# Kernel optimization log

Hardware: AMD Instinct MI355X
Metric: run time of the kernel (lower is better)

Reference implementation:

```python
import jax, jax.numpy as jnp
import numpy as np

EPS = 1e-8
LN_EPS = 1e-5
TOPK = 8

B, N, D = 8, 2048, 512


def setup_inputs() -> dict:
    key = jax.random.key(0)
    ks = jax.random.split(key, 4)
    feats = jax.random.normal(ks[0], (B, N, D), dtype=jnp.float32)
    mask = jnp.ones((B, N), dtype=bool)
    # per-layer GCN weights (no bias) and LayerNorm params, plus output LN
    W1 = jax.random.normal(ks[1], (D, D), dtype=jnp.float32) / np.sqrt(D)
    W2 = jax.random.normal(ks[2], (D, D), dtype=jnp.float32) / np.sqrt(D)
    ln1_g = jnp.ones((D,), jnp.float32); ln1_b = jnp.zeros((D,), jnp.float32)
    ln2_g = jnp.ones((D,), jnp.float32); ln2_b = jnp.zeros((D,), jnp.float32)
    out_g = jnp.ones((D,), jnp.float32); out_b = jnp.zeros((D,), jnp.float32)
    return {"feats": feats, "mask": mask, "W1": W1, "ln1_g": ln1_g, "ln1_b": ln1_b,
            "W2": W2, "ln2_g": ln2_g, "ln2_b": ln2_b, "out_g": out_g, "out_b": out_b}


def _layer_norm(x, g, b):
    mu = jnp.mean(x, axis=-1, keepdims=True)
    var = jnp.mean(jnp.square(x - mu), axis=-1, keepdims=True)
    return (x - mu) * jax.lax.rsqrt(var + LN_EPS) * g + b


def build_similarity_graph(feats, mask):
    b, n, _ = feats.shape
    mask_f = mask.astype(feats.dtype)                       # [B,N]
    valid_pair = mask[:, None, :] & mask[:, :, None]        # [B,N,N]
    vp_f = valid_pair.astype(feats.dtype)
    # cosine similarity mapped to [0,1]
    fn = feats / jnp.clip(jnp.linalg.norm(feats, axis=-1, keepdims=True), EPS)
    sim = (jnp.einsum('bnd,bmd->bnm', fn, fn) + 1.0) * 0.5
    sim = sim * vp_f
    eye = jnp.eye(n, dtype=bool)
    sim_wo_self = jnp.where(eye[None], 0.0, sim)
    # top-k neighbors per node (invalid pairs pushed to -1)
    k = min(TOPK, n - 1)
    candidate = jnp.where(valid_pair, sim_wo_self, -1.0)
    values, indices = jax.lax.top_k(candidate, k)           # [B,N,k]
    bi = jnp.arange(b)[:, None, None]
    ri = jnp.arange(n)[None, :, None]
    knn_mask = jnp.zeros((b, n, n), dtype=bool).at[bi, ri, indices].set(values > 0)
    adj = sim_wo_self * knn_mask.astype(feats.dtype)
    # symmetrize, add valid self-loops, re-mask
    adj = 0.5 * (adj + jnp.swapaxes(adj, 1, 2))
    adj = adj + jnp.eye(n, dtype=feats.dtype)[None] * (mask_f[:, :, None] * mask_f[:, None, :])
    adj = adj * vp_f
    # symmetric degree normalization
    deg_inv_sqrt = jnp.clip(adj.sum(-1), EPS) ** -0.5       # [B,N]
    adj_norm = adj * deg_inv_sqrt[:, :, None] * deg_inv_sqrt[:, None, :]
    return adj_norm * vp_f


def _gcn_layer(x, adj_norm, W, g, b, mask_f):
    out = jnp.einsum('bnm,bmd->bnd', adj_norm, x @ W) + x   # residual (Identity proj)
    out = jax.nn.relu(_layer_norm(out, g, b))
    return out * mask_f[..., None]


def reference(feats, mask, W1, ln1_g, ln1_b, W2, ln2_g, ln2_b, out_g, out_b):
    mask_f = mask.astype(feats.dtype)
    x = feats * mask_f[..., None]                           # input_proj = Identity, then mask
    adj_norm = build_similarity_graph(feats, mask)
    x = _gcn_layer(x, adj_norm, W1, ln1_g, ln1_b, mask_f)
    x = _gcn_layer(x, adj_norm, W2, ln2_g, ln2_b, mask_f)
    x = _layer_norm(x, out_g, out_b)
    return x * mask_f[..., None]
```

## Files before the change

kernel.cpp:

```cpp
#include <hip/hip_runtime.h>
#include <cstdint>


constexpr int Bb   = 8;
constexpr int Nn   = 2048;
constexpr int Dd   = 512;
constexpr int BN   = Bb * Nn;
constexpr int KTOP = 8;
constexpr int CAP  = 56;
constexpr int NSLICE = 8;

typedef __attribute__((ext_vector_type(8))) __bf16 bf16x8;
typedef __attribute__((ext_vector_type(4))) __bf16 bf16x4;
typedef __attribute__((ext_vector_type(4))) float  f32x4;

__device__ __forceinline__ void gload16(const void* g, void* l) {
  __builtin_amdgcn_global_load_lds((const __attribute__((address_space(1))) unsigned int*)g,
                                   (__attribute__((address_space(3))) unsigned int*)l,
                                   16, 0, 0);
}
__device__ __forceinline__ void barrier_raw() {
  asm volatile("" ::: "memory");
  __builtin_amdgcn_s_barrier();
  asm volatile("" ::: "memory");
}
__device__ __forceinline__ unsigned umax_(unsigned a, unsigned b) { return a > b ? a : b; }
__device__ __forceinline__ unsigned umin_(unsigned a, unsigned b) { return a > b ? b : a; }

__global__ __launch_bounds__(256) void prep_kernel(const float* __restrict__ feats,
                                                   float* __restrict__ rinv,
                                                   float* __restrict__ normv,
                                                   __bf16* __restrict__ Hk,
                                                   int* __restrict__ ecnt,
                                                   const float* __restrict__ W1,
                                                   const float* __restrict__ W2,
                                                   __bf16* __restrict__ Wk1,
                                                   __bf16* __restrict__ Wk2) {
  __shared__ float tile[64][65];
  __shared__ float rsh[64];
  const int t = threadIdx.x;

  if (blockIdx.x >= 256) {
    const int idx = blockIdx.x - 256;
    const float* W = (idx >> 8) ? W2 : W1;
    __bf16* Wk     = (idx >> 8) ? Wk2 : Wk1;
    const int rem = idx & 255;
    const int bx = (rem & 15) * 32, by = (rem >> 4) * 32;
    float (*tt)[33] = (float(*)[33])tile;
    const int lx = t & 31, ly = t >> 5;
#pragma unroll
    for (int r = 0; r < 32; r += 8)
      tt[ly + r][lx] = W[(size_t)(by + ly + r) * Dd + bx + lx];
    __syncthreads();
    if (t < 128) {
      const int k8l = t >> 5, nl = t & 31;
      bf16x8 v;
#pragma unroll
      for (int e = 0; e < 8; ++e) v[e] = (__bf16)tt[k8l * 8 + e][nl];
      *(bf16x8*)(Wk + ((size_t)((by >> 3) + k8l) * Dd + bx + nl) * 8) = v;
    }
    return;
  }

  const int r0 = blockIdx.x * 64;
  const int bz = r0 >> 11;
  const int n0 = r0 & 2047;
  const int wv = t >> 6, lane = t & 63;

  if (t < 64) ecnt[r0 + t] = 0;

  for (int i = 0; i < 16; ++i) {
    const int row = wv * 16 + i;
    const float* p = feats + (size_t)(r0 + row) * Dd + lane * 8;
    float4 a = *(const float4*)p;
    float4 b = *(const float4*)(p + 4);
    float s = a.x*a.x + a.y*a.y + a.z*a.z + a.w*a.w
            + b.x*b.x + b.y*b.y + b.z*b.z + b.w*b.w;
#pragma unroll
    for (int o = 32; o; o >>= 1) s += __shfl_down(s, o);
    if (lane == 0) {
      const float nr = fmaxf(sqrtf(s), 1e-8f);
      rsh[row] = 1.0f / nr;
      rinv[r0 + row]  = 1.0f / nr;
      normv[r0 + row] = nr;
    }
  }

  for (int kt = 0; kt < 8; ++kt) {
    __syncthreads();
#pragma unroll
    for (int p = 0; p < 4; ++p) {
      const int row = p * 16 + (t >> 4), ch = t & 15;
      float4 v = *(const float4*)(feats + (size_t)(r0 + row) * Dd + kt * 64 + ch * 4);
      tile[row][ch * 4 + 0] = v.x; tile[row][ch * 4 + 1] = v.y;
      tile[row][ch * 4 + 2] = v.z; tile[row][ch * 4 + 3] = v.w;
    }
    __syncthreads();
#pragma unroll
    for (int h = 0; h < 2; ++h) {
      const int c = h * 256 + t;
      const int k8l = c >> 6, row = c & 63;
      const float s = rsh[row];
      bf16x8 hv;
#pragma unroll
      for (int e = 0; e < 8; ++e) hv[e] = (__bf16)(tile[row][k8l * 8 + e] * s);
      *(bf16x8*)(Hk + ((size_t)(bz * 64) + (size_t)(kt * 8 + k8l)) * (Nn * 8)
                    + (n0 + row) * 8) = hv;
    }
  }
}

__device__ __forceinline__ void ins8t(float (&tv)[8], int (&ti)[8], float v, int idx) {
#pragma unroll
  for (int q = 0; q < 8; ++q) {
    bool sw = (v > tv[q]) || (v == tv[q] && idx < ti[q]);
    float a = sw ? tv[q] : v;
    int   c = sw ? ti[q] : idx;
    tv[q] = sw ? v   : tv[q];
    ti[q] = sw ? idx : ti[q];
    v = a; idx = c;
  }
}

__device__ __forceinline__ void gemm_core(const __bf16* __restrict__ Ab, int Astr, int mloc,
                                          const __bf16* __restrict__ Wk, int m0, int n0,
                                          __bf16* __restrict__ Yb, int tid, char* smem) {
  const int lane   = tid & 63;
  const int lane15 = tid & 15;
  const int kgrp   = (tid >> 4) & 3;
  const int wv     = tid >> 6;
  const int wrow0  = wv * 32;

  auto stage = [&](int t, int buf) {
    const int k80 = t << 2;
#pragma unroll
    for (int i = 0; i < 4; ++i) {
      const int c = (wv << 2) + i;
      const bool isB = c >= 8;
      const int cc = isB ? c - 8 : c;
      const int kg = cc >> 1, rb = cc & 1;
      const __bf16* g = isB
          ? Wk + ((size_t)(k80 + kg) * Dd + n0 + rb * 64 + lane) * 8
          : Ab + ((size_t)(k80 + kg) * Astr + mloc + rb * 64 + lane) * 8;
      gload16(g, smem + buf * 16384 + (isB ? 8192 : 0) + kg * 2048 + (rb * 64 + lane) * 16);
    }
  };

  f32x4 acc[2][8];
  const f32x4 z = {0.f, 0.f, 0.f, 0.f};
#pragma unroll
  for (int i = 0; i < 2; ++i)
#pragma unroll
    for (int j = 0; j < 8; ++j) acc[i][j] = z;

  stage(0, 0);
  for (int t = 0; t < 16; ++t) {
    const int cur = t & 1;
    if (t + 1 < 16) {
      stage(t + 1, cur ^ 1);
      asm volatile("s_waitcnt vmcnt(4)" ::: "memory");
    } else {
      asm volatile("s_waitcnt vmcnt(0)" ::: "memory");
    }
    barrier_raw();

    const char* sb = smem + cur * 16384;
    const int a0o = kgrp * 2048 + (wrow0 + lane15) * 16;
    bf16x8 a0 = *(const bf16x8*)(sb + a0o);
    bf16x8 a1 = *(const bf16x8*)(sb + a0o + 256);
#pragma unroll
    for (int cs = 0; cs < 8; ++cs) {
      bf16x8 b = *(const bf16x8*)(sb + 8192 + kgrp * 2048 + (cs * 16 + lane15) * 16);
      acc[0][cs] = __builtin_amdgcn_mfma_f32_16x16x32_bf16(b, a0, acc[0][cs], 0, 0, 0);
      acc[1][cs] = __builtin_amdgcn_mfma_f32_16x16x32_bf16(b, a1, acc[1][cs], 0, 0, 0);
    }
    barrier_raw();
  }
#pragma unroll
  for (int rs = 0; rs < 2; ++rs) {
    const int row = m0 + wv * 32 + rs * 16 + lane15;
#pragma unroll
    for (int cs = 0; cs < 8; ++cs) {
      bf16x4 o;
#pragma unroll
      for (int e = 0; e < 4; ++e) o[e] = (__bf16)acc[rs][cs][e];
      *(bf16x4*)(Yb + (size_t)row * Dd + n0 + cs * 16 + kgrp * 4) = o;
    }
  }
}

__global__ __launch_bounds__(256, 4) void sim_gemm_kernel(const __bf16* __restrict__ Hk,
                                                          const __bf16* __restrict__ Wk1,
                                                          __bf16* __restrict__ Yb,
                                                          float* __restrict__ pv,
                                                          int* __restrict__ pi) {
  __shared__ __align__(16) char smem[32768];
  const int tid = threadIdx.x;

  if (blockIdx.x < 512) {
    const int gb = blockIdx.x;
    const int m0 = (gb >> 2) * 128, n0 = (gb & 3) * 128;
    const __bf16* Ab = Hk + (size_t)((m0 >> 11) * 64) * (Nn * 8);
    gemm_core(Ab, Nn, m0 & 2047, Wk1, m0, n0, Yb, tid, smem);
    return;
  }

  const int f     = blockIdx.x - 512;
  const int bz    = f & 7;
  const int rr    = f >> 3;
  const int r0    = (rr & 15) * 128;
  const int slice = rr >> 4;

  const int lane   = tid & 63;
  const int lane15 = tid & 15;
  const int kgrp   = (tid >> 4) & 3;
  const int wv     = tid >> 6;
  const int wrow0  = wv * 32;
  const int bN     = bz * Nn;

  const __bf16* Hb = Hk + (size_t)(bz * 64) * (Nn * 8);

  unsigned t8k[2][8];
#pragma unroll
  for (int rs = 0; rs < 2; ++rs)
#pragma unroll
    for (int q = 0; q < 8; ++q) t8k[rs][q] = 0u;

  auto stage = [&](int t, int buf) {
    const int ct = t >> 4, k80 = (t & 15) << 2;
    const int c0 = slice * 256 + ct * 128;
#pragma unroll
    for (int i = 0; i < 4; ++i) {
      const int c = (wv << 2) + i;
      const bool isB = c >= 8;
      const int cc = isB ? c - 8 : c;
      const int kg = cc >> 1, rb = cc & 1;
      const int rbase = (isB ? c0 : r0) + rb * 64 + lane;
      gload16(Hb + ((size_t)(k80 + kg) * Nn + rbase) * 8,
              smem + buf * 16384 + (isB ? 8192 : 0) + kg * 2048 + (rb * 64 + lane) * 16);
    }
  };

  f32x4 acc[2][8];
  const f32x4 z = {0.f, 0.f, 0.f, 0.f};

  stage(0, 0);
  for (int t = 0; t < 32; ++t) {
    const int cur = t & 1;
    if ((t & 15) == 0) {
#pragma unroll
      for (int i = 0; i < 2; ++i)
#pragma unroll
        for (int j = 0; j < 8; ++j) acc[i][j] = z;
    }
    if (t + 1 < 32) {
      stage(t + 1, cur ^ 1);
      asm volatile("s_waitcnt vmcnt(4)" ::: "memory");
    } else {
      asm volatile("s_waitcnt vmcnt(0)" ::: "memory");
    }
    barrier_raw();

    const char* sb = smem + cur * 16384;
    const int a0o = kgrp * 2048 + (wrow0 + lane15) * 16;
    bf16x8 ah0 = *(const bf16x8*)(sb + a0o);
    bf16x8 ah1 = *(const bf16x8*)(sb + a0o + 256);
#pragma unroll
    for (int cs = 0; cs < 8; ++cs) {
      bf16x8 bh = *(const bf16x8*)(sb + 8192 + kgrp * 2048 + (cs * 16 + lane15) * 16);
      acc[0][cs] = __builtin_amdgcn_mfma_f32_16x16x32_bf16(bh, ah0, acc[0][cs], 0, 0, 0);
      acc[1][cs] = __builtin_amdgcn_mfma_f32_16x16x32_bf16(bh, ah1, acc[1][cs], 0, 0, 0);
    }
    barrier_raw();

    if ((t & 15) == 15) {
      const int ctile0 = slice * 256 + (t >> 4) * 128;
#pragma unroll
      for (int rs = 0; rs < 2; ++rs) {
        const int rowg = r0 + wrow0 + rs * 16 + lane15;
#pragma unroll
        for (int cs = 0; cs < 8; ++cs) {
          const int colb = ctile0 + cs * 16 + kgrp * 4;
#pragma unroll
          for (int e = 0; e < 4; ++e) {
            const int col = colb + e;
            unsigned key = (__float_as_uint(acc[rs][cs][e] + 2.0f) & 0xFFFFF800u)
                         | (unsigned)(0x7FF - col);
            key = (col == rowg) ? 0u : key;
#pragma unroll
            for (int q = 0; q < 8; ++q) {
              const unsigned hi = umax_(t8k[rs][q], key);
              key = umin_(t8k[rs][q], key);
              t8k[rs][q] = hi;
            }
          }
        }
      }
    }
  }

#pragma unroll
  for (int rs = 0; rs < 2; ++rs) {
#pragma unroll
    for (int m = 16; m <= 32; m <<= 1) {
      unsigned ok[8];
#pragma unroll
      for (int q = 0; q < 8; ++q) ok[q] = (unsigned)__shfl_xor((int)t8k[rs][q], m);
#pragma unroll
      for (int q = 0; q < 8; ++q) {
        unsigned key = ok[q];
#pragma unroll
        for (int p = 0; p < 8; ++p) {
          const unsigned hi = umax_(t8k[rs][p], key);
          key = umin_(t8k[rs][p], key);
          t8k[rs][p] = hi;
        }
      }
    }
  }

  if (lane < 16) {
#pragma unroll
    for (int rs = 0; rs < 2; ++rs) {
      const int prow = bN + r0 + wrow0 + rs * 16 + lane15;
#pragma unroll
      for (int q = 0; q < 8; ++q) {
        const unsigned key = t8k[rs][q];
        const int col = 0x7FF - (int)(key & 0x7FFu);
        const float raw = __uint_as_float(key & 0xFFFFF800u) - 2.0f;
        pv[((size_t)prow * NSLICE + slice) * 8 + q] = fmaxf((raw + 1.0f) * 0.5f, 0.0f);
        pi[((size_t)prow * NSLICE + slice) * 8 + q] = bN + col;
      }
    }
  }
}

__global__ __launch_bounds__(256, 4) void gemm2_kernel(const __bf16* __restrict__ Ak,
                                                       const __bf16* __restrict__ Wk,
                                                       __bf16* __restrict__ Yb) {
  __shared__ __align__(16) char smem[32768];
  const int gb = blockIdx.x;
  const int m0 = (gb >> 2) * 128, n0 = (gb & 3) * 128;
  gemm_core(Ak, BN, m0, Wk, m0, n0, Yb, threadIdx.x, smem);
}

__global__ __launch_bounds__(256) void refine_edges(const float* __restrict__ feats,
                                                    const float* __restrict__ rinv,
                                                    const float* __restrict__ pv,
                                                    const int* __restrict__ pi,
                                                    int* __restrict__ ecnt,
                                                    int* __restrict__ eidx,
                                                    float* __restrict__ ew) {
  const int f  = blockIdx.x;
  const int bz = f & 7;
  const int wv = threadIdx.x >> 6;
  const int lane = threadIdx.x & 63;
  const int bN = bz * Nn;
  const int row = bN + (f >> 3) * 4 + wv;

  const float scr = pv[(size_t)row * 64 + lane];
  const int   sid = pi[(size_t)row * 64 + lane];
  unsigned key = (__float_as_uint(scr) & 0xFFFFF800u) | (unsigned)(0x7FF - (sid - bN));

  const float* xi = feats + (size_t)row * Dd + lane * 8;
  const float4 xi0 = *(const float4*)xi;
  const float4 xi1 = *(const float4*)(xi + 4);
  const float  ri  = rinv[row];

  int ridx[12];
#pragma unroll
  for (int c = 0; c < 12; ++c) {
    unsigned m = key;
#pragma unroll
    for (int o = 32; o; o >>= 1) {
      const unsigned om = __shfl_xor(m, o);
      m = om > m ? om : m;
    }
    if (key == m) key = 0u;
    ridx[c] = bN + (0x7FF - (int)(m & 0x7FFu));
  }

  float rv[12];
#pragma unroll
  for (int c = 0; c < 12; c += 2) {
    const float* xa = feats + (size_t)ridx[c]     * Dd + lane * 8;
    const float* xb = feats + (size_t)ridx[c + 1] * Dd + lane * 8;
    const float4 a0 = *(const float4*)xa;
    const float4 a1 = *(const float4*)(xa + 4);
    const float4 b0 = *(const float4*)xb;
    const float4 b1 = *(const float4*)(xb + 4);
    float da = xi0.x*a0.x + xi0.y*a0.y + xi0.z*a0.z + xi0.w*a0.w
             + xi1.x*a1.x + xi1.y*a1.y + xi1.z*a1.z + xi1.w*a1.w;
    float db = xi0.x*b0.x + xi0.y*b0.y + xi0.z*b0.z + xi0.w*b0.w
             + xi1.x*b1.x + xi1.y*b1.y + xi1.z*b1.z + xi1.w*b1.w;
#pragma unroll
    for (int o = 32; o; o >>= 1) { da += __shfl_xor(da, o); db += __shfl_xor(db, o); }
    rv[c]     = (da * ri * rinv[ridx[c]]     + 1.0f) * 0.5f;
    rv[c + 1] = (db * ri * rinv[ridx[c + 1]] + 1.0f) * 0.5f;
  }

  float t8v[8]; int t8i[8];
#pragma unroll
  for (int q = 0; q < 8; ++q) { t8v[q] = -1.0f; t8i[q] = 0x7fffffff; }
#pragma unroll
  for (int c = 0; c < 12; ++c) ins8t(t8v, t8i, rv[c], ridx[c]);

  if (lane == 0) {
#pragma unroll
    for (int q = 0; q < KTOP; ++q) {
      if (t8v[q] > 0.0f) {
        const int j = t8i[q];
        const float w = 0.5f * t8v[q];
        int p = atomicAdd(&ecnt[row], 1);
        if (p < CAP) { eidx[row * CAP + p] = j; ew[row * CAP + p] = w; }
        int q2 = atomicAdd(&ecnt[j], 1);
        if (q2 < CAP) { eidx[j * CAP + q2] = row; ew[j * CAP + q2] = w; }
      }
    }
  }
}

__global__ __launch_bounds__(256) void deg_kernel(const int* __restrict__ ecnt,
                                                  const float* __restrict__ ew,
                                                  const float* __restrict__ normv,
                                                  float* __restrict__ dis,
                                                  float* __restrict__ dn) {
  const int r = blockIdx.x * 256 + threadIdx.x;
  if (r >= BN) return;
  const int cnt = min(ecnt[r], CAP);
  float d = 1.0f;
  for (int e = 0; e < cnt; ++e) d += ew[r * CAP + e];
  const float di = rsqrtf(fmaxf(d, 1e-8f));
  dis[r] = di;
  dn[r]  = di * normv[r];
}

__device__ __forceinline__ void breduce2_128(float& s, float& q, float* red) {
#pragma unroll
  for (int o = 32; o; o >>= 1) { s += __shfl_down(s, o); q += __shfl_down(q, o); }
  __syncthreads();
  if ((threadIdx.x & 63) == 0) {
    red[(threadIdx.x >> 6) * 2]     = s;
    red[(threadIdx.x >> 6) * 2 + 1] = q;
  }
  __syncthreads();
  s = red[0] + red[2];
  q = red[1] + red[3];
}

template <bool FINAL>
__global__ __launch_bounds__(128) void agg_ln_kernel(const __bf16* __restrict__ yb,
                                                     const float* __restrict__ xres_f,
                                                     const __bf16* __restrict__ xres_k,
                                                     const int* __restrict__ ecnt,
                                                     const int* __restrict__ eidx,
                                                     const float* __restrict__ ew,
                                                     const float* __restrict__ dis,
                                                     const float* __restrict__ dwv,
                                                     const float* __restrict__ g1,
                                                     const float* __restrict__ b1v,
                                                     const float* __restrict__ g2,
                                                     const float* __restrict__ b2v,
                                                     float* __restrict__ outf,
                                                     __bf16* __restrict__ outk) {
  __shared__ float red[4];
  const int row = (blockIdx.x & 7) * Nn + (blockIdx.x >> 3);
  const int tid = threadIdx.x;
  const int d0 = tid * 4;
  const float di = dis[row];
  const float swt = di * dwv[row];

  bf16x4 yv = *(const bf16x4*)(yb + (size_t)row * Dd + d0);
  float a[4];
#pragma unroll
  for (int e2 = 0; e2 < 4; ++e2) a[e2] = swt * (float)yv[e2];

  const int cnt = min(ecnt[row], CAP);
  int e = 0;
  for (; e + 4 <= cnt; e += 4) {
    const int j0 = eidx[row * CAP + e];
    const int j1 = eidx[row * CAP + e + 1];
    const int j2 = eidx[row * CAP + e + 2];
    const int j3 = eidx[row * CAP + e + 3];
    const float c0 = ew[row * CAP + e]     * di * dwv[j0];
    const float c1 = ew[row * CAP + e + 1] * di * dwv[j1];
    const float c2 = ew[row * CAP + e + 2] * di * dwv[j2];
    const float c3 = ew[row * CAP + e + 3] * di * dwv[j3];
    bf16x4 v0 = *(const bf16x4*)(yb + (size_t)j0 * Dd + d0);
    bf16x4 v1 = *(const bf16x4*)(yb + (size_t)j1 * Dd + d0);
    bf16x4 v2 = *(const bf16x4*)(yb + (size_t)j2 * Dd + d0);
    bf16x4 v3 = *(const bf16x4*)(yb + (size_t)j3 * Dd + d0);
#pragma unroll
    for (int e2 = 0; e2 < 4; ++e2)
      a[e2] += c0 * (float)v0[e2] + c1 * (float)v1[e2]
             + c2 * (float)v2[e2] + c3 * (float)v3[e2];
  }
  for (; e < cnt; ++e) {
    const int j = eidx[row * CAP + e];
    const float c = ew[row * CAP + e] * di * dwv[j];
    bf16x4 v = *(const bf16x4*)(yb + (size_t)j * Dd + d0);
#pragma unroll
    for (int e2 = 0; e2 < 4; ++e2) a[e2] += c * (float)v[e2];
  }

  if (FINAL) {
    bf16x4 u = *(const bf16x4*)(xres_k + ((size_t)(tid >> 1) * BN + row) * 8 + (tid & 1) * 4);
#pragma unroll
    for (int e2 = 0; e2 < 4; ++e2) a[e2] += (float)u[e2];
  } else {
    float4 xv = *(const float4*)(xres_f + (size_t)row * Dd + d0);
    a[0] += xv.x; a[1] += xv.y; a[2] += xv.z; a[3] += xv.w;
  }

  float s = a[0] + a[1] + a[2] + a[3];
  float qq = a[0]*a[0] + a[1]*a[1] + a[2]*a[2] + a[3]*a[3];
  breduce2_128(s, qq, red);
  const float mu = s * (1.0f / Dd);
  const float var = qq * (1.0f / Dd) - mu * mu;
  const float rs = rsqrtf(var + 1e-5f);
  float4 g = *(const float4*)(g1 + d0);
  float4 bb = *(const float4*)(b1v + d0);
  float tv[4];
  tv[0] = fmaxf((a[0] - mu) * rs * g.x + bb.x, 0.0f);
  tv[1] = fmaxf((a[1] - mu) * rs * g.y + bb.y, 0.0f);
  tv[2] = fmaxf((a[2] - mu) * rs * g.z + bb.z, 0.0f);
  tv[3] = fmaxf((a[3] - mu) * rs * g.w + bb.w, 0.0f);

  if (FINAL) {
    float s2 = tv[0] + tv[1] + tv[2] + tv[3];
    float q2 = tv[0]*tv[0] + tv[1]*tv[1] + tv[2]*tv[2] + tv[3]*tv[3];
    breduce2_128(s2, q2, red);
    const float mu2 = s2 * (1.0f / Dd);
    const float var2 = q2 * (1.0f / Dd) - mu2 * mu2;
    const float rs2 = rsqrtf(var2 + 1e-5f);
    float4 g2v = *(const float4*)(g2 + d0);
    float4 b2 = *(const float4*)(b2v + d0);
    float4 o;
    o.x = (tv[0] - mu2) * rs2 * g2v.x + b2.x;
    o.y = (tv[1] - mu2) * rs2 * g2v.y + b2.y;
    o.z = (tv[2] - mu2) * rs2 * g2v.z + b2.z;
    o.w = (tv[3] - mu2) * rs2 * g2v.w + b2.w;
    *(float4*)(outf + (size_t)row * Dd + d0) = o;
  } else {
    bf16x4 ov;
#pragma unroll
    for (int e2 = 0; e2 < 4; ++e2) ov[e2] = (__bf16)tv[e2];
    *(bf16x4*)(outk + ((size_t)(tid >> 1) * BN + row) * 8 + (tid & 1) * 4) = ov;
  }
}

extern "C" void kernel_launch(void* const* d_in, const int* in_sizes, int n_in,
                              void* d_out, int out_size, void* d_ws, size_t ws_size,
                              hipStream_t stream) {
  const float* feats = (const float*)d_in[0];
  const float* W1    = (const float*)d_in[2];
  const float* ln1_g = (const float*)d_in[3];
  const float* ln1_b = (const float*)d_in[4];
  const float* W2    = (const float*)d_in[5];
  const float* ln2_g = (const float*)d_in[6];
  const float* ln2_b = (const float*)d_in[7];
  const float* out_g = (const float*)d_in[8];
  const float* out_b = (const float*)d_in[9];
  float* out = (float*)d_out;

  char* w = (char*)d_ws;
  float* rinv  = (float*)w; w += (size_t)BN * 4;
  float* normv = (float*)w; w += (size_t)BN * 4;
  int*   ecnt  = (int*)w;   w += (size_t)BN * 4;
  int*   eidx  = (int*)w;   w += (size_t)BN * CAP * 4;
  float* ew    = (float*)w; w += (size_t)BN * CAP * 4;
  float* dis   = (float*)w; w += (size_t)BN * 4;
  float* dn    = (float*)w; w += (size_t)BN * 4;
  __bf16* Wk1  = (__bf16*)w; w += (size_t)Dd * Dd * 2;
  __bf16* Wk2  = (__bf16*)w; w += (size_t)Dd * Dd * 2;
  __bf16* Hk   = (__bf16*)w; w += (size_t)BN * Dd * 2;
  __bf16* Yb   = (__bf16*)w; w += (size_t)BN * Dd * 2;
  __bf16* h1k  = (__bf16*)w; w += (size_t)BN * Dd * 2;
  float* pv  = (float*)h1k;
  int*   pi  = (int*)((char*)h1k + (size_t)BN * NSLICE * 8 * 4);

  prep_kernel<<<768, 256, 0, stream>>>(feats, rinv, normv, Hk, ecnt,
                                       W1, W2, Wk1, Wk2);

  sim_gemm_kernel<<<1536, 256, 0, stream>>>(Hk, Wk1, Yb, pv, pi);

  refine_edges<<<BN / 4, 256, 0, stream>>>(feats, rinv, pv, pi, ecnt, eidx, ew);
  deg_kernel<<<BN / 256, 256, 0, stream>>>(ecnt, ew, normv, dis, dn);

  agg_ln_kernel<false><<<BN, 128, 0, stream>>>(Yb, feats, nullptr, ecnt, eidx, ew,
                                               dis, dn, ln1_g, ln1_b,
                                               nullptr, nullptr, nullptr, h1k);
  gemm2_kernel<<<512, 256, 0, stream>>>(h1k, Wk2, Yb);
  agg_ln_kernel<true><<<BN, 128, 0, stream>>>(Yb, nullptr, h1k, ecnt, eidx, ew,
                                              dis, dis, ln2_g, ln2_b,
                                              out_g, out_b, out, nullptr);
}
```

Measured before the change: 280.1 us.

## Use one wavefront per row in aggregation-LN and halve prep tile size

Measured after the change: 278.8 us. Within noise of the previous version (-0.5%).

```diff
diff --git a/kernel.cpp b/kernel.cpp
--- a/kernel.cpp
+++ b/kernel.cpp
@@ -36,17 +36,17 @@
                                                    const float* __restrict__ W2,
                                                    __bf16* __restrict__ Wk1,
                                                    __bf16* __restrict__ Wk2) {
-  __shared__ float tile[64][65];
-  __shared__ float rsh[64];
+  __shared__ float tile[32][65];
+  __shared__ float rsh[32];
   const int t = threadIdx.x;
 
-  if (blockIdx.x >= 256) {
-    const int idx = blockIdx.x - 256;
+  if (blockIdx.x >= 512) {
+    const int idx = blockIdx.x - 512;
     const float* W = (idx >> 8) ? W2 : W1;
     __bf16* Wk     = (idx >> 8) ? Wk2 : Wk1;
     const int rem = idx & 255;
     const int bx = (rem & 15) * 32, by = (rem >> 4) * 32;
-    float (*tt)[33] = (float(*)[33])tile;
+    __shared__ float tt[32][33];
     const int lx = t & 31, ly = t >> 5;
 #pragma unroll
     for (int r = 0; r < 32; r += 8)
@@ -62,15 +62,15 @@
     return;
   }
 
-  const int r0 = blockIdx.x * 64;
+  const int r0 = blockIdx.x * 32;
   const int bz = r0 >> 11;
   const int n0 = r0 & 2047;
   const int wv = t >> 6, lane = t & 63;
 
-  if (t < 64) ecnt[r0 + t] = 0;
-
-  for (int i = 0; i < 16; ++i) {
-    const int row = wv * 16 + i;
+  if (t < 32) ecnt[r0 + t] = 0;
+
+  for (int i = 0; i < 8; ++i) {
+    const int row = wv * 8 + i;
     const float* p = feats + (size_t)(r0 + row) * Dd + lane * 8;
     float4 a = *(const float4*)p;
     float4 b = *(const float4*)(p + 4);
@@ -88,18 +88,19 @@
 
   for (int kt = 0; kt < 8; ++kt) {
     __syncthreads();
-#pragma unroll
-    for (int p = 0; p < 4; ++p) {
-      const int row = p * 16 + (t >> 4), ch = t & 15;
-      float4 v = *(const float4*)(feats + (size_t)(r0 + row) * Dd + kt * 64 + ch * 4);
-      tile[row][ch * 4 + 0] = v.x; tile[row][ch * 4 + 1] = v.y;
-      tile[row][ch * 4 + 2] = v.z; tile[row][ch * 4 + 3] = v.w;
+    {
+      const int row = t >> 3, ch = t & 7;
+      const float* p = feats + (size_t)(r0 + row) * Dd + kt * 64 + ch * 8;
+      float4 v0 = *(const float4*)p;
+      float4 v1 = *(const float4*)(p + 4);
+      tile[row][ch * 8 + 0] = v0.x; tile[row][ch * 8 + 1] = v0.y;
+      tile[row][ch * 8 + 2] = v0.z; tile[row][ch * 8 + 3] = v0.w;
+      tile[row][ch * 8 + 4] = v1.x; tile[row][ch * 8 + 5] = v1.y;
+      tile[row][ch * 8 + 6] = v1.z; tile[row][ch * 8 + 7] = v1.w;
     }
     __syncthreads();
-#pragma unroll
-    for (int h = 0; h < 2; ++h) {
-      const int c = h * 256 + t;
-      const int k8l = c >> 6, row = c & 63;
+    {
+      const int k8l = t >> 5, row = t & 31;
       const float s = rsh[row];
       bf16x8 hv;
 #pragma unroll
@@ -435,21 +436,8 @@
   dn[r]  = di * normv[r];
 }
 
-__device__ __forceinline__ void breduce2_128(float& s, float& q, float* red) {
-#pragma unroll
-  for (int o = 32; o; o >>= 1) { s += __shfl_down(s, o); q += __shfl_down(q, o); }
-  __syncthreads();
-  if ((threadIdx.x & 63) == 0) {
-    red[(threadIdx.x >> 6) * 2]     = s;
-    red[(threadIdx.x >> 6) * 2 + 1] = q;
-  }
-  __syncthreads();
-  s = red[0] + red[2];
-  q = red[1] + red[3];
-}
-
 template <bool FINAL>
-__global__ __launch_bounds__(128) void agg_ln_kernel(const __bf16* __restrict__ yb,
+__global__ __launch_bounds__(256) void agg_ln_kernel(const __bf16* __restrict__ yb,
                                                      const float* __restrict__ xres_f,
                                                      const __bf16* __restrict__ xres_k,
                                                      const int* __restrict__ ecnt,
@@ -463,17 +451,20 @@
                                                      const float* __restrict__ b2v,
                                                      float* __restrict__ outf,
                                                      __bf16* __restrict__ outk) {
-  __shared__ float red[4];
-  const int row = (blockIdx.x & 7) * Nn + (blockIdx.x >> 3);
-  const int tid = threadIdx.x;
-  const int d0 = tid * 4;
+  const int bz = blockIdx.x & 7;
+  const int rr = blockIdx.x >> 3;
+  const int wv = threadIdx.x >> 6;
+  const int lane = threadIdx.x & 63;
+  const int row = bz * Nn + rr * 4 + wv;
+  const int d0 = lane * 8;
+
   const float di = dis[row];
   const float swt = di * dwv[row];
 
-  bf16x4 yv = *(const bf16x4*)(yb + (size_t)row * Dd + d0);
-  float a[4];
-#pragma unroll
-  for (int e2 = 0; e2 < 4; ++e2) a[e2] = swt * (float)yv[e2];
+  bf16x8 yv = *(const bf16x8*)(yb + (size_t)row * Dd + d0);
+  float a[8];
+#pragma unroll
+  for (int e2 = 0; e2 < 8; ++e2) a[e2] = swt * (float)yv[e2];
 
   const int cnt = min(ecnt[row], CAP);
   int e = 0;
@@ -486,66 +477,88 @@
     const float c1 = ew[row * CAP + e + 1] * di * dwv[j1];
     const float c2 = ew[row * CAP + e + 2] * di * dwv[j2];
     const float c3 = ew[row * CAP + e + 3] * di * dwv[j3];
-    bf16x4 v0 = *(const bf16x4*)(yb + (size_t)j0 * Dd + d0);
-    bf16x4 v1 = *(const bf16x4*)(yb + (size_t)j1 * Dd + d0);
-    bf16x4 v2 = *(const bf16x4*)(yb + (size_t)j2 * Dd + d0);
-    bf16x4 v3 = *(const bf16x4*)(yb + (size_t)j3 * Dd + d0);
-#pragma unroll
-    for (int e2 = 0; e2 < 4; ++e2)
+    bf16x8 v0 = *(const bf16x8*)(yb + (size_t)j0 * Dd + d0);
+    bf16x8 v1 = *(const bf16x8*)(yb + (size_t)j1 * Dd + d0);
+    bf16x8 v2 = *(const bf16x8*)(yb + (size_t)j2 * Dd + d0);
+    bf16x8 v3 = *(const bf16x8*)(yb + (size_t)j3 * Dd + d0);
+#pragma unroll
+    for (int e2 = 0; e2 < 8; ++e2)
       a[e2] += c0 * (float)v0[e2] + c1 * (float)v1[e2]
              + c2 * (float)v2[e2] + c3 * (float)v3[e2];
   }
   for (; e < cnt; ++e) {
     const int j = eidx[row * CAP + e];
     const float c = ew[row * CAP + e] * di * dwv[j];
-    bf16x4 v = *(const bf16x4*)(yb + (size_t)j * Dd + d0);
-#pragma unroll
-    for (int e2 = 0; e2 < 4; ++e2) a[e2] += c * (float)v[e2];
+    bf16x8 v = *(const bf16x8*)(yb + (size_t)j * Dd + d0);
+#pragma unroll
+    for (int e2 = 0; e2 < 8; ++e2) a[e2] += c * (float)v[e2];
   }
 
   if (FINAL) {
-    bf16x4 u = *(const bf16x4*)(xres_k + ((size_t)(tid >> 1) * BN + row) * 8 + (tid & 1) * 4);
-#pragma unroll
-    for (int e2 = 0; e2 < 4; ++e2) a[e2] += (float)u[e2];
+    bf16x8 u = *(const bf16x8*)(xres_k + ((size_t)lane * BN + row) * 8);
+#pragma unroll
+    for (int e2 = 0; e2 < 8; ++e2) a[e2] += (float)u[e2];
   } else {
-    float4 xv = *(const float4*)(xres_f + (size_t)row * Dd + d0);
-    a[0] += xv.x; a[1] += xv.y; a[2] += xv.z; a[3] += xv.w;
-  }
-
-  float s = a[0] + a[1] + a[2] + a[3];
-  float qq = a[0]*a[0] + a[1]*a[1] + a[2]*a[2] + a[3]*a[3];
-  breduce2_128(s, qq, red);
+    const float* xp = xres_f + (size_t)row * Dd + d0;
+    float4 x0 = *(const float4*)xp;
+    float4 x1 = *(const float4*)(xp + 4);
+    a[0] += x0.x; a[1] += x0.y; a[2] += x0.z; a[3] += x0.w;
+    a[4] += x1.x; a[5] += x1.y; a[6] += x1.z; a[7] += x1.w;
+  }
+
+  float s = 0.f, qq = 0.f;
+#pragma unroll
+  for (int e2 = 0; e2 < 8; ++e2) { s += a[e2]; qq += a[e2] * a[e2]; }
+#pragma unroll
+  for (int o = 32; o; o >>= 1) { s += __shfl_xor(s, o); qq += __shfl_xor(qq, o); }
   const float mu = s * (1.0f / Dd);
   const float var = qq * (1.0f / Dd) - mu * mu;
   const float rs = rsqrtf(var + 1e-5f);
-  float4 g = *(const float4*)(g1 + d0);
-  float4 bb = *(const float4*)(b1v + d0);
-  float tv[4];
-  tv[0] = fmaxf((a[0] - mu) * rs * g.x + bb.x, 0.0f);
-  tv[1] = fmaxf((a[1] - mu) * rs * g.y + bb.y, 0.0f);
-  tv[2] = fmaxf((a[2] - mu) * rs * g.z + bb.z, 0.0f);
-  tv[3] = fmaxf((a[3] - mu) * rs * g.w + bb.w, 0.0f);
+
+  const float* gp = g1 + d0;
+  const float* bp = b1v + d0;
+  float4 g0 = *(const float4*)gp,  g1v = *(const float4*)(gp + 4);
+  float4 bb0 = *(const float4*)bp, bb1 = *(const float4*)(bp + 4);
+  float tv[8];
+  tv[0] = fmaxf((a[0] - mu) * rs * g0.x + bb0.x, 0.0f);
+  tv[1] = fmaxf((a[1] - mu) * rs * g0.y + bb0.y, 0.0f);
+  tv[2] = fmaxf((a[2] - mu) * rs * g0.z + bb0.z, 0.0f);
+  tv[3] = fmaxf((a[3] - mu) * rs * g0.w + bb0.w, 0.0f);
+  tv[4] = fmaxf((a[4] - mu) * rs * g1v.x + bb1.x, 0.0f);
+  tv[5] = fmaxf((a[5] - mu) * rs * g1v.y + bb1.y, 0.0f);
+  tv[6] = fmaxf((a[6] - mu) * rs * g1v.z + bb1.z, 0.0f);
+  tv[7] = fmaxf((a[7] - mu) * rs * g1v.w + bb1.w, 0.0f);
 
   if (FINAL) {
-    float s2 = tv[0] + tv[1] + tv[2] + tv[3];
-    float q2 = tv[0]*tv[0] + tv[1]*tv[1] + tv[2]*tv[2] + tv[3]*tv[3];
-    breduce2_128(s2, q2, red);
+    float s2 = 0.f, q2 = 0.f;
+#pragma unroll
+    for (int e2 = 0; e2 < 8; ++e2) { s2 += tv[e2]; q2 += tv[e2] * tv[e2]; }
+#pragma unroll
+    for (int o = 32; o; o >>= 1) { s2 += __shfl_xor(s2, o); q2 += __shfl_xor(q2, o); }
     const float mu2 = s2 * (1.0f / Dd);
     const float var2 = q2 * (1.0f / Dd) - mu2 * mu2;
     const float rs2 = rsqrtf(var2 + 1e-5f);
-    float4 g2v = *(const float4*)(g2 + d0);
-    float4 b2 = *(const float4*)(b2v + d0);
-    float4 o;
-    o.x = (tv[0] - mu2) * rs2 * g2v.x + b2.x;
-    o.y = (tv[1] - mu2) * rs2 * g2v.y + b2.y;
-    o.z = (tv[2] - mu2) * rs2 * g2v.z + b2.z;
-    o.w = (tv[3] - mu2) * rs2 * g2v.w + b2.w;
-    *(float4*)(outf + (size_t)row * Dd + d0) = o;
+    const float* g2p = g2 + d0;
+    const float* b2p = b2v + d0;
+    float4 G0 = *(const float4*)g2p,  G1 = *(const float4*)(g2p + 4);
+    float4 B0 = *(const float4*)b2p,  B1 = *(const float4*)(b2p + 4);
+    float4 o0, o1;
+    o0.x = (tv[0] - mu2) * rs2 * G0.x + B0.x;
+    o0.y = (tv[1] - mu2) * rs2 * G0.y + B0.y;
+    o0.z = (tv[2] - mu2) * rs2 * G0.z + B0.z;
+    o0.w = (tv[3] - mu2) * rs2 * G0.w + B0.w;
+    o1.x = (tv[4] - mu2) * rs2 * G1.x + B1.x;
+    o1.y = (tv[5] - mu2) * rs2 * G1.y + B1.y;
+    o1.z = (tv[6] - mu2) * rs2 * G1.z + B1.z;
+    o1.w = (tv[7] - mu2) * rs2 * G1.w + B1.w;
+    float* op = outf + (size_t)row * Dd + d0;
+    *(float4*)op = o0;
+    *(float4*)(op + 4) = o1;
   } else {
-    bf16x4 ov;
-#pragma unroll
-    for (int e2 = 0; e2 < 4; ++e2) ov[e2] = (__bf16)tv[e2];
-    *(bf16x4*)(outk + ((size_t)(tid >> 1) * BN + row) * 8 + (tid & 1) * 4) = ov;
+    bf16x8 ov;
+#pragma unroll
+    for (int e2 = 0; e2 < 8; ++e2) ov[e2] = (__bf16)tv[e2];
+    *(bf16x8*)(outk + ((size_t)lane * BN + row) * 8) = ov;
   }
 }
 
@@ -579,19 +592,19 @@
   float* pv  = (float*)h1k;
   int*   pi  = (int*)((char*)h1k + (size_t)BN * NSLICE * 8 * 4);
 
-  prep_kernel<<<768, 256, 0, stream>>>(feats, rinv, normv, Hk, ecnt,
-                                       W1, W2, Wk1, Wk2);
+  prep_kernel<<<1024, 256, 0, stream>>>(feats, rinv, normv, Hk, ecnt,
+                                        W1, W2, Wk1, Wk2);
 
   sim_gemm_kernel<<<1536, 256, 0, stream>>>(Hk, Wk1, Yb, pv, pi);
 
   refine_edges<<<BN / 4, 256, 0, stream>>>(feats, rinv, pv, pi, ecnt, eidx, ew);
   deg_kernel<<<BN / 256, 256, 0, stream>>>(ecnt, ew, normv, dis, dn);
 
-  agg_ln_kernel<false><<<BN, 128, 0, stream>>>(Yb, feats, nullptr, ecnt, eidx, ew,
-                                               dis, dn, ln1_g, ln1_b,
-                                               nullptr, nullptr, nullptr, h1k);
+  agg_ln_kernel<false><<<BN / 4, 256, 0, stream>>>(Yb, feats, nullptr, ecnt, eidx, ew,
+                                                   dis, dn, ln1_g, ln1_b,
+                                                   nullptr, nullptr, nullptr, h1k);
   gemm2_kernel<<<512, 256, 0, stream>>>(h1k, Wk2, Yb);
-  agg_ln_kernel<true><<<BN, 128, 0, stream>>>(Yb, nullptr, h1k, ecnt, eidx, ew,
-                                              dis, dis, ln2_g, ln2_b,
-                                              out_g, out_b, out, nullptr);
-}
+  agg_ln_kernel<true><<<BN / 4, 256, 0, stream>>>(Yb, nullptr, h1k, ecnt, eidx, ew,
+                                                  dis, dis, ln2_g, ln2_b,
+                                                  out_g, out_b, out, nullptr);
+}
```
